# Optimization experiments

Hardware: AMD Instinct MI355X
Metric: run time of the kernel (lower is better)

The kernel has to match this reference:

```python
import jax, jax.numpy as jnp
import numpy as np

D_MODEL, N_LEVELS, N_HEADS, N_POINTS = 256, 4, 8, 4
HEAD_DIM = D_MODEL // N_HEADS
SPATIAL = [(100, 100), (50, 50), (25, 25), (13, 13)]  # (H, W) per level
BATCH = 2


def setup_inputs() -> dict:
    key = jax.random.key(0)
    ks = jax.random.split(key, 10)
    len_in = sum(h * w for h, w in SPATIAL)
    n, lq = BATCH, len_in
    s = 0.02
    mlp = N_HEADS * N_LEVELS * N_POINTS
    starts = np.cumsum([0] + [h * w for h, w in SPATIAL])[:-1]
    return {
        "query": jax.random.normal(ks[0], (n, lq, D_MODEL), jnp.float32),
        "reference_points": jax.random.uniform(ks[1], (n, lq, N_LEVELS, 2), jnp.float32),
        "input_flatten": jax.random.normal(ks[2], (n, len_in, D_MODEL), jnp.float32),
        "input_spatial_shapes": jnp.array(SPATIAL, dtype=jnp.int32),
        "input_level_start_index": jnp.array(starts, dtype=jnp.int32),
        "Wv": jax.random.normal(ks[3], (D_MODEL, D_MODEL), jnp.float32) * s,
        "bv": jnp.zeros((D_MODEL,), jnp.float32),
        "Woff": jax.random.normal(ks[4], (D_MODEL, mlp * 2), jnp.float32) * s,
        "boff": jax.random.normal(ks[5], (mlp * 2,), jnp.float32) * s,
        "Wattn": jax.random.normal(ks[6], (D_MODEL, mlp), jnp.float32) * s,
        "battn": jnp.zeros((mlp,), jnp.float32),
        "Wout": jax.random.normal(ks[7], (D_MODEL, D_MODEL), jnp.float32) * s,
        "bout": jnp.zeros((D_MODEL,), jnp.float32),
    }


def _ms_deform_attn_core(value, spatial_shapes, loc, aw):
    """value [N,S,M,D]; loc [N,Lq,M,L,P,2] in [0,1]; aw [N,Lq,M,L,P] -> [N,Lq,M*D].
    Faithful to F.grid_sample(mode='bilinear', padding_mode='zeros', align_corners=False)."""
    n, lq, m, L, p, _ = loc.shape
    d = value.shape[-1]
    out = jnp.zeros((n, m, lq, d), value.dtype)
    gather = jax.vmap(jax.vmap(lambda v, i: v[i]))  # vmap over N and M
    start = 0
    for lvl, (H, W) in enumerate(spatial_shapes):
        v = value[:, start:start + H * W].transpose(0, 2, 1, 3)  # [N,M,HW,D]
        start += H * W
        # align_corners=False: grid g=2*loc-1 -> pixel = ((g+1)*size-1)/2 = loc*size-0.5
        x = loc[:, :, :, lvl, :, 0] * W - 0.5  # [N,Lq,M,P]
        y = loc[:, :, :, lvl, :, 1] * H - 0.5
        x0 = jnp.floor(x)
        y0 = jnp.floor(y)
        wx = x - x0
        wy = y - y0
        x0i = x0.astype(jnp.int32)
        y0i = y0.astype(jnp.int32)
        samp = jnp.zeros((n, m, lq * p, d), value.dtype)
        for dy, wyc in ((0, 1.0 - wy), (1, wy)):
            for dx, wxc in ((0, 1.0 - wx), (1, wx)):
                xi = x0i + dx
                yi = y0i + dy
                valid = (xi >= 0) & (xi < W) & (yi >= 0) & (yi < H)  # zeros padding
                idx = jnp.clip(yi, 0, H - 1) * W + jnp.clip(xi, 0, W - 1)
                idx = idx.transpose(0, 2, 1, 3).reshape(n, m, lq * p)
                w = (wxc * wyc * valid).transpose(0, 2, 1, 3).reshape(n, m, lq * p)
                samp = samp + gather(v, idx) * w[..., None]
        samp = samp.reshape(n, m, lq, p, d)
        aw_l = aw[:, :, :, lvl, :].transpose(0, 2, 1, 3)  # [N,M,Lq,P]
        out = out + (samp * aw_l[..., None]).sum(3)
    return out.transpose(0, 2, 1, 3).reshape(n, lq, m * d)


def reference(query, reference_points, input_flatten, input_spatial_shapes,
              input_level_start_index, Wv, bv, Woff, boff, Wattn, battn, Wout, bout):
    n, lq, _ = query.shape
    m, L, p = N_HEADS, N_LEVELS, N_POINTS
    shapes = np.asarray(input_spatial_shapes)  # concrete/static [L,2] = (H,W)
    value = (input_flatten @ Wv + bv).reshape(n, -1, m, HEAD_DIM)
    off = (query @ Woff + boff).reshape(n, lq, m, L, p, 2)
    aw = jax.nn.softmax((query @ Wattn + battn).reshape(n, lq, m, L * p), axis=-1)
    aw = aw.reshape(n, lq, m, L, p)
    norm = jnp.asarray(shapes[:, ::-1].astype(np.float32))  # [L,2] = (W,H)
    loc = reference_points[:, :, None, :, None, :] + off / norm[None, None, None, :, None, :]
    out = _ms_deform_attn_core(value, [tuple(s) for s in shapes.tolist()], loc, aw)
    return out @ Wout + bout
```

## Files before the change

### kernel.cpp

```cpp
#include <hip/hip_runtime.h>
#include <hip/hip_bf16.h>

#define NB    2
#define LQ    13294
#define DM    256
#define NH    8
#define HD    32
#define NL    4
#define NP    4
#define ROWS  (NB*LQ)

#define OFF_VALUE 0u
#define OFF_TMP   13613056u
#define OFF_OFFS  27226112u
#define OFF_AWL   54452224u
#define OFF_WT    61258752u
#define OFF_FLAG  61717504u

#define WT_WV    0
#define WT_WOFF  65536
#define WT_WATTN 131072
#define WT_WOUT  163840

typedef __attribute__((ext_vector_type(8))) short short8;
typedef __attribute__((ext_vector_type(4))) float floatx4;

static __device__ __forceinline__ float blo(int u)  { return __uint_as_float(((unsigned)u) << 16); }
static __device__ __forceinline__ float bhif(int u) { return __uint_as_float(((unsigned)u) & 0xffff0000u); }

static __device__ __forceinline__ int pack_bf2(float a, float b) {
    __hip_bfloat162 h(__float2bfloat16(a), __float2bfloat16(b));
    int u; __builtin_memcpy(&u, &h, 4); return u;
}

static __device__ __forceinline__ float load_bias(const void* b, int i, int flag) {
    return flag ? __bfloat162float(((const __hip_bfloat16*)b)[i]) : ((const float*)b)[i];
}

static __device__ __forceinline__ void gload_lds16(const void* g, void* l) {
    __builtin_amdgcn_global_load_lds(
        (const __attribute__((address_space(1))) unsigned*)g,
        (__attribute__((address_space(3))) unsigned*)l, 16, 0, 0);
}

__global__ void sniff_k(const unsigned int* __restrict__ q, int* __restrict__ flag) {
    const int t = threadIdx.x;
    int hits = 0;
#pragma unroll
    for (int i = 0; i < 4; ++i) {
        unsigned lo = q[t * 4 + i] & 0xffffu;
        unsigned e  = (lo >> 7) & 0xffu;
        if ((e >= 110u && e <= 132u) || lo == 0u) ++hits;
    }
#pragma unroll
    for (int s = 1; s < 64; s <<= 1) hits += __shfl_xor(hits, s);
    if (t == 0) *flag = (hits > 160) ? 1 : 0;
}

__global__ __launch_bounds__(256) void trans_k(
    const void* __restrict__ s0, const void* __restrict__ s1,
    const void* __restrict__ s2, const void* __restrict__ s3,
    short* __restrict__ wt, const int* __restrict__ flagp)
{
    const int flag = *flagp;
    const int z = blockIdx.z;
    const void* src = (z == 0) ? s0 : (z == 1) ? s1 : (z == 2) ? s2 : s3;
    short* dst = wt + ((z == 0) ? WT_WV : (z == 1) ? WT_WOFF : (z == 2) ? WT_WATTN : WT_WOUT);
    const int N = (z == 2) ? 128 : 256;
    const int n0 = blockIdx.x * 32, k0 = blockIdx.y * 32;
    if (n0 >= N) return;

    __shared__ short tile[32 * 36];
    const int t = threadIdx.x;
    const int r = t >> 3, c4 = (t & 7) * 4;
    if (flag) {
        const short* sp = (const short*)src + (k0 + r) * N + n0 + c4;
        *(short4*)&tile[r * 36 + c4] = *(const short4*)sp;
    } else {
        const float* sp = (const float*)src + (k0 + r) * N + n0 + c4;
        float4 v = *(const float4*)sp;
        short4 o;
        o.x = (short)(pack_bf2(v.x, v.x) & 0xffff);
        o.y = (short)(pack_bf2(v.y, v.y) & 0xffff);
        o.z = (short)(pack_bf2(v.z, v.z) & 0xffff);
        o.w = (short)(pack_bf2(v.w, v.w) & 0xffff);
        *(short4*)&tile[r * 36 + c4] = o;
    }
    __syncthreads();
    const int nn = t >> 3, r4 = (t & 7) * 4;
    short4 o;
    o.x = tile[(r4 + 0) * 36 + nn];
    o.y = tile[(r4 + 1) * 36 + nn];
    o.z = tile[(r4 + 2) * 36 + nn];
    o.w = tile[(r4 + 3) * 36 + nn];
    *(short4*)&dst[(n0 + nn) * 256 + k0 + r4] = o;
}

__global__ __launch_bounds__(256) void gemm_front_k(
    const void* __restrict__ flat, const void* __restrict__ query,
    const short* __restrict__ wt,
    const void* __restrict__ bv, const void* __restrict__ boff, const void* __restrict__ battn,
    short* __restrict__ value, float* __restrict__ offsb, short* __restrict__ awl,
    const int* __restrict__ flagp)
{
    const int  flag = *flagp;
    const bool a_bf = (flag != 0);

    __shared__ __align__(16) short Bs[128 * 256];
    __shared__ __align__(16) short As[2][128 * 32];

    const int tid = threadIdx.x;
    const int w = tid >> 6, lane = tid & 63;
    const int qd = lane >> 4, ln = lane & 15;
    const int bx = blockIdx.x;
    const bool isv = (bx < 2);
    const void*  A   = isv ? flat : query;
    const short* Wtb = isv ? (wt + WT_WV) : (wt + WT_WOFF);
    const int colbase = (isv ? bx : bx - 2) * 128;
    const int bm = blockIdx.y * 128;

#pragma unroll
    for (int r = 0; r < 16; ++r) {
        const int c = r * 256 + tid;
        const int col = c >> 5;
        const int kc = (c & 31) ^ (col & 31);
        gload_lds16(Wtb + (colbase + col) * 256 + kc * 8, &Bs[(r * 256 + w * 64) * 8]);
    }

    auto stage_a = [&](int buf, int k0) {
#pragma unroll
        for (int r = 0; r < 2; ++r) {
            const int c = r * 256 + tid;
            const int row = min(bm + (c >> 2), ROWS - 1);
            const int kc = ((c & 3) ^ ((c >> 2) & 3)) * 8;
            if (a_bf) {
                gload_lds16((const short*)A + row * 256 + k0 + kc,
                            &As[buf][(r * 256 + w * 64) * 8]);
            } else {
                const float* p = (const float*)A + row * 256 + k0 + kc;
                float4 f0 = *(const float4*)p, f1 = *(const float4*)(p + 4);
                int4 pk; pk.x = pack_bf2(f0.x, f0.y); pk.y = pack_bf2(f0.z, f0.w);
                         pk.z = pack_bf2(f1.x, f1.y); pk.w = pack_bf2(f1.z, f1.w);
                *(int4*)&As[buf][c * 8] = pk;
            }
        }
    };
    stage_a(0, 0);
    __syncthreads();

    const int wm = (w & 1) * 64, wn = (w >> 1) * 64;

    floatx4 acc[4][4];
#pragma unroll
    for (int i = 0; i < 4; ++i)
#pragma unroll
        for (int j = 0; j < 4; ++j) acc[i][j] = floatx4{0.f, 0.f, 0.f, 0.f};

#pragma unroll
    for (int i0 = 0; i0 < 8; ++i0) {
        if (i0 < 7) stage_a((i0 + 1) & 1, 32 * (i0 + 1));
        const short* Ab = As[i0 & 1];
        short8 af[4], bf[4];
#pragma unroll
        for (int i = 0; i < 4; ++i) {
            const int row = wm + i * 16 + ln;
            af[i] = *(const short8*)&Ab[(row * 4 + (qd ^ (row & 3))) * 8];
        }
#pragma unroll
        for (int j = 0; j < 4; ++j) {
            const int col = wn + j * 16 + ln;
            bf[j] = *(const short8*)&Bs[(col * 32 + ((4 * i0 + qd) ^ (col & 31))) * 8];
        }
#pragma unroll
        for (int i = 0; i < 4; ++i)
#pragma unroll
            for (int j = 0; j < 4; ++j)
                acc[i][j] = __builtin_amdgcn_mfma_f32_16x16x32_bf16(af[i], bf[j], acc[i][j], 0, 0, 0);
        if (i0 < 7) __syncthreads();
    }

#pragma unroll
    for (int j = 0; j < 4; ++j) {
        const int col = colbase + wn + j * 16 + ln;
        float bj;
        if (isv)            bj = load_bias(bv, col, flag);
        else if (col < 256) bj = load_bias(boff, col, flag);
        else                bj = load_bias(battn, col - 256, flag);
#pragma unroll
        for (int i = 0; i < 4; ++i) {
#pragma unroll
            for (int r = 0; r < 4; ++r) {
                const int row = bm + wm + i * 16 + qd * 4 + r;
                if (row >= ROWS) continue;
                const float v = acc[i][j][r] + bj;
                if (isv)            value[row * 256 + col] = (short)(pack_bf2(v, v) & 0xffff);
                else if (col < 256) offsb[row * 256 + col] = v;
                else                awl[row * 128 + col - 256] = (short)(pack_bf2(v, v) & 0xffff);
            }
        }
    }
}

__global__ __launch_bounds__(256) void gemm_out_k(
    const short* __restrict__ tmp, const short* __restrict__ wtout,
    const void* __restrict__ bout, void* __restrict__ C,
    const int* __restrict__ flagp)
{
    const int flag = *flagp;

    __shared__ __align__(16) short Bs[128 * 256];
    __shared__ __align__(16) short As[2][128 * 32];

    const int tid = threadIdx.x;
    const int w = tid >> 6, lane = tid & 63;
    const int qd = lane >> 4, ln = lane & 15;
    const int colbase = blockIdx.x * 128;
    const int bm = blockIdx.y * 128;

#pragma unroll
    for (int r = 0; r < 16; ++r) {
        const int c = r * 256 + tid;
        const int col = c >> 5;
        const int kc = (c & 31) ^ (col & 31);
        gload_lds16(wtout + (colbase + col) * 256 + kc * 8, &Bs[(r * 256 + w * 64) * 8]);
    }

    auto stage_a = [&](int buf, int k0) {
#pragma unroll
        for (int r = 0; r < 2; ++r) {
            const int c = r * 256 + tid;
            const int row = min(bm + (c >> 2), ROWS - 1);
            const int kc = ((c & 3) ^ ((c >> 2) & 3)) * 8;
            gload_lds16(tmp + row * 256 + k0 + kc, &As[buf][(r * 256 + w * 64) * 8]);
        }
    };
    stage_a(0, 0);
    __syncthreads();

    const int wm = (w & 1) * 64, wn = (w >> 1) * 64;

    floatx4 acc[4][4];
#pragma unroll
    for (int i = 0; i < 4; ++i)
#pragma unroll
        for (int j = 0; j < 4; ++j) acc[i][j] = floatx4{0.f, 0.f, 0.f, 0.f};

#pragma unroll
    for (int i0 = 0; i0 < 8; ++i0) {
        if (i0 < 7) stage_a((i0 + 1) & 1, 32 * (i0 + 1));
        const short* Ab = As[i0 & 1];
        short8 af[4], bf[4];
#pragma unroll
        for (int i = 0; i < 4; ++i) {
            const int row = wm + i * 16 + ln;
            af[i] = *(const short8*)&Ab[(row * 4 + (qd ^ (row & 3))) * 8];
        }
#pragma unroll
        for (int j = 0; j < 4; ++j) {
            const int col = wn + j * 16 + ln;
            bf[j] = *(const short8*)&Bs[(col * 32 + ((4 * i0 + qd) ^ (col & 31))) * 8];
        }
#pragma unroll
        for (int i = 0; i < 4; ++i)
#pragma unroll
            for (int j = 0; j < 4; ++j)
                acc[i][j] = __builtin_amdgcn_mfma_f32_16x16x32_bf16(af[i], bf[j], acc[i][j], 0, 0, 0);
        if (i0 < 7) __syncthreads();
    }

#pragma unroll
    for (int j = 0; j < 4; ++j) {
        const int col = colbase + wn + j * 16 + ln;
        const float bj = load_bias(bout, col, flag);
#pragma unroll
        for (int i = 0; i < 4; ++i) {
#pragma unroll
            for (int r = 0; r < 4; ++r) {
                const int row = bm + wm + i * 16 + qd * 4 + r;
                if (row >= ROWS) continue;
                const float v = acc[i][j][r] + bj;
                if (flag) ((__hip_bfloat16*)C)[row * 256 + col] = __float2bfloat16(v);
                else      ((float*)C)[row * 256 + col] = v;
            }
        }
    }
}

__global__ __launch_bounds__(256) void sampler_k(
    const void* __restrict__ refp, const short* __restrict__ value,
    const float* __restrict__ offs, const short* __restrict__ awl,
    short* __restrict__ tmp, const int* __restrict__ flagp)
{
    const int flag = *flagp;
    const int nq = blockIdx.x * 4 + (threadIdx.x >> 6);
    const int lane = threadIdx.x & 63;
    const int h = lane >> 3, u = lane & 7;
    const int n = (nq >= LQ) ? 1 : 0;

    const int lg = *(const int*)(awl + nq * 128 + h * 16 + u * 2);
    float l0 = blo(lg), l1 = bhif(lg);
    float m = fmaxf(l0, l1);
    m = fmaxf(m, __shfl_xor(m, 1));
    m = fmaxf(m, __shfl_xor(m, 2));
    m = fmaxf(m, __shfl_xor(m, 4));
    float e0 = __expf(l0 - m), e1 = __expf(l1 - m);
    float s = e0 + e1;
    s += __shfl_xor(s, 1);
    s += __shfl_xor(s, 2);
    s += __shfl_xor(s, 4);
    const float inv = 1.f / s;
    const float w0 = e0 * inv, w1 = e1 * inv;

    const float4 of = *(const float4*)(offs + nq * 256 + h * 32 + u * 4);

    float rxl, ryl;
    if (flag) {
        const int rr = *(const int*)((const short*)refp + nq * 8 + (u & 3) * 2);
        rxl = blo(rr); ryl = bhif(rr);
    } else {
        const float* rp = (const float*)refp + nq * 8 + (u & 3) * 2;
        rxl = rp[0]; ryl = rp[1];
    }

    const short* vb = value + (n ? LQ * 256 : 0) + h * 32 + u * 4;

    float a0 = 0.f, a1 = 0.f, a2 = 0.f, a3 = 0.f;

    const int WlA[NL] = {100, 50, 25, 13};
    const int StA[NL] = {0, 10000, 12500, 13125};

#pragma unroll
    for (int idx = 0; idx < 16; ++idx) {
        const int l = idx >> 2;
        const int Wl = WlA[l];
        const float Wf = (float)Wl;
        const int owner = h * 8 + (idx >> 1);
        const float ox = __shfl((idx & 1) ? of.z : of.x, owner);
        const float oy = __shfl((idx & 1) ? of.w : of.y, owner);
        const float wa = __shfl((idx & 1) ? w1 : w0, owner);
        const float rx = __shfl(rxl, h * 8 + l);
        const float ry = __shfl(ryl, h * 8 + l);

        const float px = fmaf(rx, Wf, ox) - 0.5f;
        const float py = fmaf(ry, Wf, oy) - 0.5f;
        const float x0f = floorf(px), y0f = floorf(py);
        const float wx = px - x0f, wy = py - y0f;
        const int x0 = (int)x0f, y0 = (int)y0f;
        const short* vl = vb + StA[l] * 256;

#pragma unroll
        for (int dy = 0; dy < 2; ++dy) {
#pragma unroll
            for (int dx = 0; dx < 2; ++dx) {
                const int xi = x0 + dx, yi = y0 + dy;
                const bool vld = (xi >= 0) & (xi < Wl) & (yi >= 0) & (yi < Wl);
                const float wgt = (dx ? wx : 1.f - wx) * (dy ? wy : 1.f - wy);
                const float ww = vld ? wa * wgt : 0.f;
                const int xc = min(max(xi, 0), Wl - 1);
                const int yc = min(max(yi, 0), Wl - 1);
                const int2 raw = *(const int2*)(vl + (yc * Wl + xc) * 256);
                a0 = fmaf(ww, blo(raw.x),  a0);
                a1 = fmaf(ww, bhif(raw.x), a1);
                a2 = fmaf(ww, blo(raw.y),  a2);
                a3 = fmaf(ww, bhif(raw.y), a3);
            }
        }
    }

    int2 o;
    o.x = pack_bf2(a0, a1);
    o.y = pack_bf2(a2, a3);
    *(int2*)(tmp + nq * 256 + h * 32 + u * 4) = o;
}

extern "C" void kernel_launch(void* const* d_in, const int* in_sizes, int n_in,
                              void* d_out, int out_size, void* d_ws, size_t ws_size,
                              hipStream_t stream)
{
    const void* query  = d_in[0];
    const void* refpts = d_in[1];
    const void* flat   = d_in[2];
    const void* Wv     = d_in[5];
    const void* bv     = d_in[6];
    const void* Woff   = d_in[7];
    const void* boff   = d_in[8];
    const void* Wattn  = d_in[9];
    const void* battn  = d_in[10];
    const void* Wout   = d_in[11];
    const void* bout   = d_in[12];

    char* ws = (char*)d_ws;
    short* value = (short*)(ws + OFF_VALUE);
    short* tmp   = (short*)(ws + OFF_TMP);
    float* offsb = (float*)(ws + OFF_OFFS);
    short* awl   = (short*)(ws + OFF_AWL);
    short* wt    = (short*)(ws + OFF_WT);
    int*   flagp = (int*)(ws + OFF_FLAG);

    const int gmy = (ROWS + 127) / 128;

    sniff_k<<<1, 64, 0, stream>>>((const unsigned int*)query, flagp);
    trans_k<<<dim3(8, 8, 4), 256, 0, stream>>>(Wv, Woff, Wattn, Wout, wt, flagp);
    gemm_front_k<<<dim3(5, gmy), 256, 0, stream>>>(flat, query, wt, bv, boff, battn,
                                                   value, offsb, awl, flagp);
    sampler_k<<<ROWS / 4, 256, 0, stream>>>(refpts, value, offsb, awl, tmp, flagp);
    gemm_out_k<<<dim3(2, gmy), 256, 0, stream>>>(tmp, wt + WT_WOUT, bout, d_out, flagp);
}
```

Before: 252.4 us.

## Restructure GEMMs to direct A loads with two M-tiles, bf16 offsets, redistributed sampler

Both GEMM kernels drop the LDS-staged, double-buffered A path and read A fragments directly from global memory. Each block now processes two 128-row tiles so the padded LDS copy of B is reused, and the grid shrinks to 104 rows. The sampling offsets are stored as bf16 instead of fp32, halving that intermediate buffer. The sampler is reorganised so each lane computes the corner positions and weights for its own two points, then broadcasts them across the head group with shuffles. The risks are more latency exposed on uncoalesced A loads, reduced occupancy, and lower precision in the offsets.

New measurement: 298.8 us. 1.18x slower.

```diff
diff --git a/kernel.cpp b/kernel.cpp
--- a/kernel.cpp
+++ b/kernel.cpp
@@ -11,17 +11,19 @@
 #define ROWS  (NB*LQ)
 
 #define OFF_VALUE 0u
-#define OFF_TMP   13613056u
-#define OFF_OFFS  27226112u
-#define OFF_AWL   54452224u
-#define OFF_WT    61258752u
-#define OFF_FLAG  61717504u
+#define OFF_OFFS  13613056u
+#define OFF_AWL   27226112u
+#define OFF_TMP   34032640u
+#define OFF_WT    47645696u
+#define OFF_FLAG  48104448u
 
 #define WT_WV    0
 #define WT_WOFF  65536
 #define WT_WATTN 131072
 #define WT_WOUT  163840
 
+#define BSTR 264
+
 typedef __attribute__((ext_vector_type(8))) short short8;
 typedef __attribute__((ext_vector_type(4))) float floatx4;
 
@@ -37,10 +39,16 @@
     return flag ? __bfloat162float(((const __hip_bfloat16*)b)[i]) : ((const float*)b)[i];
 }
 
-static __device__ __forceinline__ void gload_lds16(const void* g, void* l) {
-    __builtin_amdgcn_global_load_lds(
-        (const __attribute__((address_space(1))) unsigned*)g,
-        (__attribute__((address_space(3))) unsigned*)l, 16, 0, 0);
+static __device__ __forceinline__ short8 load_afrag(const void* A, int row, int k, bool a_bf) {
+    if (a_bf) {
+        return *(const short8*)((const short*)A + row * 256 + k);
+    } else {
+        const float* p = (const float*)A + row * 256 + k;
+        float4 f0 = *(const float4*)p, f1 = *(const float4*)(p + 4);
+        int4 pk; pk.x = pack_bf2(f0.x, f0.y); pk.y = pack_bf2(f0.z, f0.w);
+                 pk.z = pack_bf2(f1.x, f1.y); pk.w = pack_bf2(f1.z, f1.w);
+        short8 r; __builtin_memcpy(&r, &pk, 16); return r;
+    }
 }
 
 __global__ void sniff_k(const unsigned int* __restrict__ q, int* __restrict__ flag) {
@@ -100,102 +108,80 @@
     const void* __restrict__ flat, const void* __restrict__ query,
     const short* __restrict__ wt,
     const void* __restrict__ bv, const void* __restrict__ boff, const void* __restrict__ battn,
-    short* __restrict__ value, float* __restrict__ offsb, short* __restrict__ awl,
+    short* __restrict__ value, short* __restrict__ offsb, short* __restrict__ awl,
     const int* __restrict__ flagp)
 {
     const int  flag = *flagp;
     const bool a_bf = (flag != 0);
 
-    __shared__ __align__(16) short Bs[128 * 256];
-    __shared__ __align__(16) short As[2][128 * 32];
+    __shared__ __align__(16) short Bs[128 * BSTR];
 
     const int tid = threadIdx.x;
-    const int w = tid >> 6, lane = tid & 63;
-    const int qd = lane >> 4, ln = lane & 15;
     const int bx = blockIdx.x;
     const bool isv = (bx < 2);
     const void*  A   = isv ? flat : query;
     const short* Wtb = isv ? (wt + WT_WV) : (wt + WT_WOFF);
     const int colbase = (isv ? bx : bx - 2) * 128;
-    const int bm = blockIdx.y * 128;
-
-#pragma unroll
-    for (int r = 0; r < 16; ++r) {
-        const int c = r * 256 + tid;
-        const int col = c >> 5;
-        const int kc = (c & 31) ^ (col & 31);
-        gload_lds16(Wtb + (colbase + col) * 256 + kc * 8, &Bs[(r * 256 + w * 64) * 8]);
-    }
-
-    auto stage_a = [&](int buf, int k0) {
-#pragma unroll
-        for (int r = 0; r < 2; ++r) {
-            const int c = r * 256 + tid;
-            const int row = min(bm + (c >> 2), ROWS - 1);
-            const int kc = ((c & 3) ^ ((c >> 2) & 3)) * 8;
-            if (a_bf) {
-                gload_lds16((const short*)A + row * 256 + k0 + kc,
-                            &As[buf][(r * 256 + w * 64) * 8]);
-            } else {
-                const float* p = (const float*)A + row * 256 + k0 + kc;
-                float4 f0 = *(const float4*)p, f1 = *(const float4*)(p + 4);
-                int4 pk; pk.x = pack_bf2(f0.x, f0.y); pk.y = pack_bf2(f0.z, f0.w);
-                         pk.z = pack_bf2(f1.x, f1.y); pk.w = pack_bf2(f1.z, f1.w);
-                *(int4*)&As[buf][c * 8] = pk;
-            }
-        }
-    };
-    stage_a(0, 0);
+
+#pragma unroll
+    for (int i = 0; i < 16; ++i) {
+        const int ch = i * 256 + tid;
+        const int col = ch >> 5, ks = (ch & 31) * 8;
+        *(int4*)&Bs[col * BSTR + ks] = *(const int4*)(Wtb + (colbase + col) * 256 + ks);
+    }
     __syncthreads();
 
+    const int w = tid >> 6, lane = tid & 63;
+    const int qd = lane >> 4, ln = lane & 15;
     const int wm = (w & 1) * 64, wn = (w >> 1) * 64;
 
-    floatx4 acc[4][4];
-#pragma unroll
-    for (int i = 0; i < 4; ++i)
-#pragma unroll
-        for (int j = 0; j < 4; ++j) acc[i][j] = floatx4{0.f, 0.f, 0.f, 0.f};
-
-#pragma unroll
-    for (int i0 = 0; i0 < 8; ++i0) {
-        if (i0 < 7) stage_a((i0 + 1) & 1, 32 * (i0 + 1));
-        const short* Ab = As[i0 & 1];
-        short8 af[4], bf[4];
-#pragma unroll
-        for (int i = 0; i < 4; ++i) {
-            const int row = wm + i * 16 + ln;
-            af[i] = *(const short8*)&Ab[(row * 4 + (qd ^ (row & 3))) * 8];
-        }
+    for (int mi = 0; mi < 2; ++mi) {
+        const int bm = (blockIdx.y * 2 + mi) * 128;
+
+        floatx4 acc[4][4];
+#pragma unroll
+        for (int i = 0; i < 4; ++i)
+#pragma unroll
+            for (int j = 0; j < 4; ++j) acc[i][j] = floatx4{0.f, 0.f, 0.f, 0.f};
+
+#pragma unroll
+        for (int k0 = 0; k0 < 256; k0 += 32) {
+            const int kk = k0 + qd * 8;
+            short8 af[4], bf[4];
+#pragma unroll
+            for (int i = 0; i < 4; ++i) {
+                const int row = min(bm + wm + i * 16 + ln, ROWS - 1);
+                af[i] = load_afrag(A, row, kk, a_bf);
+            }
+#pragma unroll
+            for (int j = 0; j < 4; ++j)
+                bf[j] = *(const short8*)&Bs[(wn + j * 16 + ln) * BSTR + kk];
+#pragma unroll
+            for (int i = 0; i < 4; ++i)
+#pragma unroll
+                for (int j = 0; j < 4; ++j)
+                    acc[i][j] = __builtin_amdgcn_mfma_f32_16x16x32_bf16(af[i], bf[j], acc[i][j], 0, 0, 0);
+        }
+
 #pragma unroll
         for (int j = 0; j < 4; ++j) {
-            const int col = wn + j * 16 + ln;
-            bf[j] = *(const short8*)&Bs[(col * 32 + ((4 * i0 + qd) ^ (col & 31))) * 8];
-        }
-#pragma unroll
-        for (int i = 0; i < 4; ++i)
-#pragma unroll
-            for (int j = 0; j < 4; ++j)
-                acc[i][j] = __builtin_amdgcn_mfma_f32_16x16x32_bf16(af[i], bf[j], acc[i][j], 0, 0, 0);
-        if (i0 < 7) __syncthreads();
-    }
-
-#pragma unroll
-    for (int j = 0; j < 4; ++j) {
-        const int col = colbase + wn + j * 16 + ln;
-        float bj;
-        if (isv)            bj = load_bias(bv, col, flag);
-        else if (col < 256) bj = load_bias(boff, col, flag);
-        else                bj = load_bias(battn, col - 256, flag);
-#pragma unroll
-        for (int i = 0; i < 4; ++i) {
-#pragma unroll
-            for (int r = 0; r < 4; ++r) {
-                const int row = bm + wm + i * 16 + qd * 4 + r;
-                if (row >= ROWS) continue;
-                const float v = acc[i][j][r] + bj;
-                if (isv)            value[row * 256 + col] = (short)(pack_bf2(v, v) & 0xffff);
-                else if (col < 256) offsb[row * 256 + col] = v;
-                else                awl[row * 128 + col - 256] = (short)(pack_bf2(v, v) & 0xffff);
+            const int col = colbase + wn + j * 16 + ln;
+            float bj;
+            if (isv)            bj = load_bias(bv, col, flag);
+            else if (col < 256) bj = load_bias(boff, col, flag);
+            else                bj = load_bias(battn, col - 256, flag);
+#pragma unroll
+            for (int i = 0; i < 4; ++i) {
+#pragma unroll
+                for (int r = 0; r < 4; ++r) {
+                    const int row = bm + wm + i * 16 + qd * 4 + r;
+                    if (row >= ROWS) continue;
+                    const float v = acc[i][j][r] + bj;
+                    const short hv = (short)(pack_bf2(v, v) & 0xffff);
+                    if (isv)            value[row * 256 + col] = hv;
+                    else if (col < 256) offsb[row * 256 + col] = hv;
+                    else                awl[row * 128 + col - 256] = hv;
+                }
             }
         }
     }
@@ -207,80 +193,65 @@
     const int* __restrict__ flagp)
 {
     const int flag = *flagp;
-
-    __shared__ __align__(16) short Bs[128 * 256];
-    __shared__ __align__(16) short As[2][128 * 32];
+    __shared__ __align__(16) short Bs[128 * BSTR];
 
     const int tid = threadIdx.x;
+    const int colbase = blockIdx.x * 128;
+
+#pragma unroll
+    for (int i = 0; i < 16; ++i) {
+        const int ch = i * 256 + tid;
+        const int col = ch >> 5, ks = (ch & 31) * 8;
+        *(int4*)&Bs[col * BSTR + ks] = *(const int4*)(wtout + (colbase + col) * 256 + ks);
+    }
+    __syncthreads();
+
     const int w = tid >> 6, lane = tid & 63;
     const int qd = lane >> 4, ln = lane & 15;
-    const int colbase = blockIdx.x * 128;
-    const int bm = blockIdx.y * 128;
-
-#pragma unroll
-    for (int r = 0; r < 16; ++r) {
-        const int c = r * 256 + tid;
-        const int col = c >> 5;
-        const int kc = (c & 31) ^ (col & 31);
-        gload_lds16(wtout + (colbase + col) * 256 + kc * 8, &Bs[(r * 256 + w * 64) * 8]);
-    }
-
-    auto stage_a = [&](int buf, int k0) {
-#pragma unroll
-        for (int r = 0; r < 2; ++r) {
-            const int c = r * 256 + tid;
-            const int row = min(bm + (c >> 2), ROWS - 1);
-            const int kc = ((c & 3) ^ ((c >> 2) & 3)) * 8;
-            gload_lds16(tmp + row * 256 + k0 + kc, &As[buf][(r * 256 + w * 64) * 8]);
-        }
-    };
-    stage_a(0, 0);
-    __syncthreads();
-
     const int wm = (w & 1) * 64, wn = (w >> 1) * 64;
 
-    floatx4 acc[4][4];
-#pragma unroll
-    for (int i = 0; i < 4; ++i)
-#pragma unroll
-        for (int j = 0; j < 4; ++j) acc[i][j] = floatx4{0.f, 0.f, 0.f, 0.f};
-
-#pragma unroll
-    for (int i0 = 0; i0 < 8; ++i0) {
-        if (i0 < 7) stage_a((i0 + 1) & 1, 32 * (i0 + 1));
-        const short* Ab = As[i0 & 1];
-        short8 af[4], bf[4];
-#pragma unroll
-        for (int i = 0; i < 4; ++i) {
-            const int row = wm + i * 16 + ln;
-            af[i] = *(const short8*)&Ab[(row * 4 + (qd ^ (row & 3))) * 8];
-        }
+    for (int mi = 0; mi < 2; ++mi) {
+        const int bm = (blockIdx.y * 2 + mi) * 128;
+
+        floatx4 acc[4][4];
+#pragma unroll
+        for (int i = 0; i < 4; ++i)
+#pragma unroll
+            for (int j = 0; j < 4; ++j) acc[i][j] = floatx4{0.f, 0.f, 0.f, 0.f};
+
+#pragma unroll
+        for (int k0 = 0; k0 < 256; k0 += 32) {
+            const int kk = k0 + qd * 8;
+            short8 af[4], bf[4];
+#pragma unroll
+            for (int i = 0; i < 4; ++i) {
+                const int row = min(bm + wm + i * 16 + ln, ROWS - 1);
+                af[i] = *(const short8*)(tmp + row * 256 + kk);
+            }
+#pragma unroll
+            for (int j = 0; j < 4; ++j)
+                bf[j] = *(const short8*)&Bs[(wn + j * 16 + ln) * BSTR + kk];
+#pragma unroll
+            for (int i = 0; i < 4; ++i)
+#pragma unroll
+                for (int j = 0; j < 4; ++j)
+                    acc[i][j] = __builtin_amdgcn_mfma_f32_16x16x32_bf16(af[i], bf[j], acc[i][j], 0, 0, 0);
+        }
+
 #pragma unroll
         for (int j = 0; j < 4; ++j) {
-            const int col = wn + j * 16 + ln;
-            bf[j] = *(const short8*)&Bs[(col * 32 + ((4 * i0 + qd) ^ (col & 31))) * 8];
-        }
-#pragma unroll
-        for (int i = 0; i < 4; ++i)
-#pragma unroll
-            for (int j = 0; j < 4; ++j)
-                acc[i][j] = __builtin_amdgcn_mfma_f32_16x16x32_bf16(af[i], bf[j], acc[i][j], 0, 0, 0);
-        if (i0 < 7) __syncthreads();
-    }
-
-#pragma unroll
-    for (int j = 0; j < 4; ++j) {
-        const int col = colbase + wn + j * 16 + ln;
-        const float bj = load_bias(bout, col, flag);
-#pragma unroll
-        for (int i = 0; i < 4; ++i) {
-#pragma unroll
-            for (int r = 0; r < 4; ++r) {
-                const int row = bm + wm + i * 16 + qd * 4 + r;
-                if (row >= ROWS) continue;
-                const float v = acc[i][j][r] + bj;
-                if (flag) ((__hip_bfloat16*)C)[row * 256 + col] = __float2bfloat16(v);
-                else      ((float*)C)[row * 256 + col] = v;
+            const int col = colbase + wn + j * 16 + ln;
+            const float bj = load_bias(bout, col, flag);
+#pragma unroll
+            for (int i = 0; i < 4; ++i) {
+#pragma unroll
+                for (int r = 0; r < 4; ++r) {
+                    const int row = bm + wm + i * 16 + qd * 4 + r;
+                    if (row >= ROWS) continue;
+                    const float v = acc[i][j][r] + bj;
+                    if (flag) ((__hip_bfloat16*)C)[row * 256 + col] = __float2bfloat16(v);
+                    else      ((float*)C)[row * 256 + col] = v;
+                }
             }
         }
     }
@@ -288,13 +259,14 @@
 
 __global__ __launch_bounds__(256) void sampler_k(
     const void* __restrict__ refp, const short* __restrict__ value,
-    const float* __restrict__ offs, const short* __restrict__ awl,
+    const short* __restrict__ offs, const short* __restrict__ awl,
     short* __restrict__ tmp, const int* __restrict__ flagp)
 {
     const int flag = *flagp;
     const int nq = blockIdx.x * 4 + (threadIdx.x >> 6);
     const int lane = threadIdx.x & 63;
     const int h = lane >> 3, u = lane & 7;
+    const int gbase = lane & ~7;
     const int n = (nq >= LQ) ? 1 : 0;
 
     const int lg = *(const int*)(awl + nq * 128 + h * 16 + u * 2);
@@ -311,7 +283,9 @@
     const float inv = 1.f / s;
     const float w0 = e0 * inv, w1 = e1 * inv;
 
-    const float4 of = *(const float4*)(offs + nq * 256 + h * 32 + u * 4);
+    const int2 ow = *(const int2*)(offs + nq * 256 + h * 32 + u * 4);
+    const float ox0 = blo(ow.x), oy0 = bhif(ow.x);
+    const float ox1 = blo(ow.y), oy1 = bhif(ow.y);
 
     float rxl, ryl;
     if (flag) {
@@ -321,44 +295,49 @@
         const float* rp = (const float*)refp + nq * 8 + (u & 3) * 2;
         rxl = rp[0]; ryl = rp[1];
     }
-
-    const short* vb = value + (n ? LQ * 256 : 0) + h * 32 + u * 4;
-
+    const int lvl = u >> 1;
+    const float rx = __shfl(rxl, gbase + lvl);
+    const float ry = __shfl(ryl, gbase + lvl);
+    const int Wl = (lvl == 0) ? 100 : (lvl == 1) ? 50 : (lvl == 2) ? 25 : 13;
+    const int St = (lvl == 0) ? 0 : (lvl == 1) ? 10000 : (lvl == 2) ? 12500 : 13125;
+    const float Wf = (float)Wl;
+
+    const int vbase = (n ? LQ * 256 : 0) + h * 32 + u * 4;
     float a0 = 0.f, a1 = 0.f, a2 = 0.f, a3 = 0.f;
 
-    const int WlA[NL] = {100, 50, 25, 13};
-    const int StA[NL] = {0, 10000, 12500, 13125};
-
-#pragma unroll
-    for (int idx = 0; idx < 16; ++idx) {
-        const int l = idx >> 2;
-        const int Wl = WlA[l];
-        const float Wf = (float)Wl;
-        const int owner = h * 8 + (idx >> 1);
-        const float ox = __shfl((idx & 1) ? of.z : of.x, owner);
-        const float oy = __shfl((idx & 1) ? of.w : of.y, owner);
-        const float wa = __shfl((idx & 1) ? w1 : w0, owner);
-        const float rx = __shfl(rxl, h * 8 + l);
-        const float ry = __shfl(ryl, h * 8 + l);
-
+#pragma unroll
+    for (int p = 0; p < 2; ++p) {
+        const float ox = p ? ox1 : ox0;
+        const float oy = p ? oy1 : oy0;
+        const float wa = p ? w1 : w0;
         const float px = fmaf(rx, Wf, ox) - 0.5f;
         const float py = fmaf(ry, Wf, oy) - 0.5f;
         const float x0f = floorf(px), y0f = floorf(py);
         const float wx = px - x0f, wy = py - y0f;
         const int x0 = (int)x0f, y0 = (int)y0f;
-        const short* vl = vb + StA[l] * 256;
-
-#pragma unroll
-        for (int dy = 0; dy < 2; ++dy) {
-#pragma unroll
-            for (int dx = 0; dx < 2; ++dx) {
-                const int xi = x0 + dx, yi = y0 + dy;
-                const bool vld = (xi >= 0) & (xi < Wl) & (yi >= 0) & (yi < Wl);
-                const float wgt = (dx ? wx : 1.f - wx) * (dy ? wy : 1.f - wy);
-                const float ww = vld ? wa * wgt : 0.f;
-                const int xc = min(max(xi, 0), Wl - 1);
-                const int yc = min(max(yi, 0), Wl - 1);
-                const int2 raw = *(const int2*)(vl + (yc * Wl + xc) * 256);
+
+        int   pofs[4];
+        float wcn[4];
+#pragma unroll
+        for (int c = 0; c < 4; ++c) {
+            const int dx = c & 1, dy = c >> 1;
+            const int xi = x0 + dx, yi = y0 + dy;
+            const bool vld = (xi >= 0) & (xi < Wl) & (yi >= 0) & (yi < Wl);
+            const float wgt = (dx ? wx : 1.f - wx) * (dy ? wy : 1.f - wy);
+            wcn[c] = vld ? wa * wgt : 0.f;
+            const int xc = min(max(xi, 0), Wl - 1);
+            const int yc = min(max(yi, 0), Wl - 1);
+            pofs[c] = (St + yc * Wl + xc) * 256;
+        }
+
+#pragma unroll
+        for (int sIdx = 0; sIdx < 8; ++sIdx) {
+            const int src = gbase + sIdx;
+#pragma unroll
+            for (int c = 0; c < 4; ++c) {
+                const int   po = __shfl(pofs[c], src);
+                const float ww = __shfl(wcn[c], src);
+                const int2 raw = *(const int2*)(value + vbase + po);
                 a0 = fmaf(ww, blo(raw.x),  a0);
                 a1 = fmaf(ww, bhif(raw.x), a1);
                 a2 = fmaf(ww, blo(raw.y),  a2);
@@ -391,18 +370,16 @@
 
     char* ws = (char*)d_ws;
     short* value = (short*)(ws + OFF_VALUE);
-    short* tmp   = (short*)(ws + OFF_TMP);
-    float* offsb = (float*)(ws + OFF_OFFS);
+    short* offsb = (short*)(ws + OFF_OFFS);
     short* awl   = (short*)(ws + OFF_AWL);
+    short* tmpb  = (short*)(ws + OFF_TMP);
     short* wt    = (short*)(ws + OFF_WT);
     int*   flagp = (int*)(ws + OFF_FLAG);
 
-    const int gmy = (ROWS + 127) / 128;
-
     sniff_k<<<1, 64, 0, stream>>>((const unsigned int*)query, flagp);
     trans_k<<<dim3(8, 8, 4), 256, 0, stream>>>(Wv, Woff, Wattn, Wout, wt, flagp);
-    gemm_front_k<<<dim3(5, gmy), 256, 0, stream>>>(flat, query, wt, bv, boff, battn,
+    gemm_front_k<<<dim3(5, 104), 256, 0, stream>>>(flat, query, wt, bv, boff, battn,
                                                    value, offsb, awl, flagp);
-    sampler_k<<<ROWS / 4, 256, 0, stream>>>(refpts, value, offsb, awl, tmp, flagp);
-    gemm_out_k<<<dim3(2, gmy), 256, 0, stream>>>(tmp, wt + WT_WOUT, bout, d_out, flagp);
-}
+    sampler_k<<<ROWS / 4, 256, 0, stream>>>(refpts, value, offsb, awl, tmpb, flagp);
+    gemm_out_k<<<dim3(2, 104), 256, 0, stream>>>(tmpb, wt + WT_WOUT, bout, d_out, flagp);
+}
```
